# Kernel optimization log

Measured on AMD Instinct MI355X. Metric: run time of the kernel, lower is better.

The kernel has to match this reference:

```python
import jax, jax.numpy as jnp
import numpy as np

INPUT_SIZE = 1024
HEAD_SIZE = 64


def setup_inputs() -> dict:
    key = jax.random.key(0)
    kx, kk, kq, kv = jax.random.split(key, 4)
    B, T, C, H = 4, 4096, INPUT_SIZE, HEAD_SIZE
    x = jax.random.normal(kx, (B, T, C), dtype=jnp.float32)
    # nn.Linear(C, H, bias=False) weight is (H, C); we store transposed (C, H)
    # so that y = x @ W matches torch's x @ weight.T
    scale = 1.0 / np.sqrt(C)
    Wk = jax.random.uniform(kk, (C, H), dtype=jnp.float32, minval=-scale, maxval=scale)
    Wq = jax.random.uniform(kq, (C, H), dtype=jnp.float32, minval=-scale, maxval=scale)
    Wv = jax.random.uniform(kv, (C, H), dtype=jnp.float32, minval=-scale, maxval=scale)
    return {"x": x, "Wk": Wk, "Wq": Wq, "Wv": Wv}


def reference(x, Wk, Wq, Wv):
    B, T, C = x.shape
    k = x @ Wk  # (B, T, H)
    q = x @ Wq
    v = x @ Wv
    H = k.shape[-1]
    # scaled scores (B, T, T)
    wei = jnp.einsum('bth,bsh->bts', q, k) * (H ** -0.5)
    causal = jnp.tril(jnp.ones((T, T), dtype=bool))
    wei = jnp.where(causal, wei, -jnp.inf)
    wei = jax.nn.softmax(wei, axis=-1)
    out = jnp.einsum('bts,bsh->bth', wei, v)  # (B, T, H)
    return out
```

## Files before the change

kernel.cpp:

```cpp
#include <hip/hip_runtime.h>
#include <math.h>


#define BT   16384
#define TDIM 4096
#define CDIM 1024
#define HDIM 64
#define ACCW 68
#define NSLOT 288

typedef __attribute__((ext_vector_type(8))) short bf16x8;
typedef __attribute__((ext_vector_type(4))) float f32x4;
typedef __attribute__((ext_vector_type(8))) unsigned short us8;
typedef __attribute__((ext_vector_type(4))) unsigned short us4;

static __device__ __forceinline__ unsigned short f2bf(float f) {
    unsigned int u = __float_as_uint(f);
    u += 0x7fffu + ((u >> 16) & 1u);
    return (unsigned short)(u >> 16);
}

static __device__ __forceinline__ void pswap(unsigned &x, unsigned &y) {
    asm("v_permlane32_swap_b32 %0, %1" : "+v"(x), "+v"(y));
    asm("v_permlane16_swap_b32 %0, %1" : "+v"(x), "+v"(y));
}

__global__ __launch_bounds__(256) void wtrans(
    const float* __restrict__ Wk, const float* __restrict__ Wq,
    const float* __restrict__ Wv, unsigned short* __restrict__ wtg)
{
    int idx = blockIdx.x * 256 + threadIdx.x;
    int mat = idx >> 16;
    int rem = idx & 65535;
    int h = rem >> 10, c = rem & 1023;
    const float* W = (mat == 0) ? Wk : (mat == 1) ? Wq : Wv;
    wtg[idx] = f2bf(W[c * HDIM + h]);
}

__global__ __launch_bounds__(512) void qkv_proj(
    const float* __restrict__ x, const unsigned short* __restrict__ wtg,
    unsigned short* __restrict__ kg, unsigned short* __restrict__ qg,
    unsigned short* __restrict__ vtg)
{
    __shared__ __align__(16) unsigned short xs[2][32][72];
    __shared__ __align__(16) unsigned short wts[2][192][72];
    const int t = threadIdx.x;
    const int lane = t & 63, wv = t >> 6, quad = lane >> 4, l16 = lane & 15;
    const int mt = wv >> 2;
    const int nq = wv & 3;
    const int row0 = blockIdx.x * 32;

    const int xr = t >> 4, xc4 = (t & 15) * 4;
    const int wn = t >> 3, wc8 = (t & 7) * 8;

    f32x4 acc3[3];
    #pragma unroll
    for (int i = 0; i < 3; i++) acc3[i] = (f32x4){0.f, 0.f, 0.f, 0.f};

    const size_t xrow = (size_t)(row0 + xr) * CDIM + xc4;

    float4 xq[8];
    #pragma unroll
    for (int c = 0; c < 8; c++)
        xq[c] = *(const float4*)&x[xrow + c * 64];

    us8 w0 = *(const us8*)&wtg[(size_t)(wn +   0) * CDIM + wc8];
    us8 w1 = *(const us8*)&wtg[(size_t)(wn +  64) * CDIM + wc8];
    us8 w2 = *(const us8*)&wtg[(size_t)(wn + 128) * CDIM + wc8];

    {
        us4 pk = { f2bf(xq[0].x), f2bf(xq[0].y), f2bf(xq[0].z), f2bf(xq[0].w) };
        *(us4*)&xs[0][xr][xc4] = pk;
        *(us8*)&wts[0][wn +   0][wc8] = w0;
        *(us8*)&wts[0][wn +  64][wc8] = w1;
        *(us8*)&wts[0][wn + 128][wc8] = w2;
    }
    xq[0] = *(const float4*)&x[xrow + 8 * 64];
    w0 = *(const us8*)&wtg[(size_t)(wn +   0) * CDIM + 64 + wc8];
    w1 = *(const us8*)&wtg[(size_t)(wn +  64) * CDIM + 64 + wc8];
    w2 = *(const us8*)&wtg[(size_t)(wn + 128) * CDIM + 64 + wc8];
    __syncthreads();

    #pragma unroll
    for (int it = 0; it < 16; it++) {
        const int buf = it & 1;
        if (it + 1 < 16) {
            const int sl = (it + 1) & 7;
            us4 pk = { f2bf(xq[sl].x), f2bf(xq[sl].y),
                       f2bf(xq[sl].z), f2bf(xq[sl].w) };
            *(us4*)&xs[buf ^ 1][xr][xc4] = pk;
            *(us8*)&wts[buf ^ 1][wn +   0][wc8] = w0;
            *(us8*)&wts[buf ^ 1][wn +  64][wc8] = w1;
            *(us8*)&wts[buf ^ 1][wn + 128][wc8] = w2;
            if (it + 9 < 16)
                xq[sl] = *(const float4*)&x[xrow + (it + 9) * 64];
            if (it + 2 < 16) {
                int nc = (it + 2) * 64;
                w0 = *(const us8*)&wtg[(size_t)(wn +   0) * CDIM + nc + wc8];
                w1 = *(const us8*)&wtg[(size_t)(wn +  64) * CDIM + nc + wc8];
                w2 = *(const us8*)&wtg[(size_t)(wn + 128) * CDIM + nc + wc8];
            }
        }
        bf16x8 a0 = *(const bf16x8*)&xs[buf][mt * 16 + l16][quad * 8];
        bf16x8 a1 = *(const bf16x8*)&xs[buf][mt * 16 + l16][32 + quad * 8];
        #pragma unroll
        for (int j = 0; j < 3; j++) {
            int nt = nq * 3 + j;
            bf16x8 b0 = *(const bf16x8*)&wts[buf][nt * 16 + l16][quad * 8];
            bf16x8 b1 = *(const bf16x8*)&wts[buf][nt * 16 + l16][32 + quad * 8];
            acc3[j] = __builtin_amdgcn_mfma_f32_16x16x32_bf16(a0, b0, acc3[j], 0, 0, 0);
            acc3[j] = __builtin_amdgcn_mfma_f32_16x16x32_bf16(a1, b1, acc3[j], 0, 0, 0);
        }
        __syncthreads();
    }

    const int mrow = row0 + mt * 16 + quad * 4;
    #pragma unroll
    for (int j = 0; j < 3; j++) {
        int nt = nq * 3 + j;
        int mat = nt >> 2;
        int col = (nt & 3) * 16 + l16;
        if (mat == 2) {
            int bb = mrow >> 12, tr = mrow & 4095;
            us4 pv = { f2bf(acc3[j][0]), f2bf(acc3[j][1]),
                       f2bf(acc3[j][2]), f2bf(acc3[j][3]) };
            *(us4*)&vtg[((size_t)(bb * HDIM + col) << 12) + tr] = pv;
        } else {
            float s = (mat == 1) ? 0.125f : 1.0f;
            unsigned short* dst = (mat == 0) ? kg : qg;
            #pragma unroll
            for (int reg = 0; reg < 4; reg++)
                dst[(size_t)(mrow + reg) * HDIM + col] = f2bf(acc3[j][reg] * s);
        }
    }
}

__global__ __launch_bounds__(256) void attn(
    const unsigned short* __restrict__ qg, const unsigned short* __restrict__ kg,
    const unsigned short* __restrict__ vtg, float* __restrict__ slabs)
{
    __shared__ __align__(16) unsigned short Ks[2][64][72];
    __shared__ __align__(16) unsigned short Vt[2][64][72];

    const int t = threadIdx.x;
    const int lane = t & 63, wv = t >> 6, quad = lane >> 4, l16 = lane & 15;

    const int b = blockIdx.x / NSLOT;
    const int s = blockIdx.x - b * NSLOT;
    int a;
    if      (s < 8)   a = 0;
    else if (s < 24)  a = 1;
    else if (s < 48)  a = 2;
    else if (s < 80)  a = 3;
    else if (s < 120) a = 4;
    else if (s < 168) a = 5;
    else if (s < 224) a = 6;
    else              a = 7;
    const int u  = s - 4 * a * (a + 1);
    const int qt = a * 8 + u / (a + 1);
    const int c  = u % (a + 1);

    const size_t bbase = (size_t)b * TDIM;
    const int Q0 = qt * 64;
    const int kt0 = c * 8;
    const int kt1 = (kt0 + 7 < qt) ? kt0 + 7 : qt;

    const int qrow = Q0 + wv * 16 + l16;
    const bf16x8 qa0 = *(const bf16x8*)&qg[(bbase + qrow) * HDIM + quad * 8];
    const bf16x8 qa1 = *(const bf16x8*)&qg[(bbase + qrow) * HDIM + 32 + quad * 8];

    const short onev = (l16 == 0) ? (short)0x3F80 : (short)0;
    const bf16x8 ones = { onev, onev, onev, onev, onev, onev, onev, onev };

    f32x4 O[5];
    #pragma unroll
    for (int i = 0; i < 5; i++) O[i] = (f32x4){0.f, 0.f, 0.f, 0.f};

    const int fr = t >> 3, fc = (t & 7) * 8;

    us8 kr0 = *(const us8*)&kg[(bbase + kt0 * 64 + fr) * HDIM + fc];
    us8 kr1 = *(const us8*)&kg[(bbase + kt0 * 64 + fr + 32) * HDIM + fc];
    us8 vr0 = *(const us8*)&vtg[((size_t)(b * HDIM + fr) << 12) + kt0 * 64 + fc];
    us8 vr1 = *(const us8*)&vtg[((size_t)(b * HDIM + fr + 32) << 12) + kt0 * 64 + fc];
    *(us8*)&Ks[0][fr][fc] = kr0;
    *(us8*)&Ks[0][fr + 32][fc] = kr1;
    *(us8*)&Vt[0][fr][fc] = vr0;
    *(us8*)&Vt[0][fr + 32][fc] = vr1;
    if (kt0 < kt1) {
        int kn = kt0 + 1;
        kr0 = *(const us8*)&kg[(bbase + kn * 64 + fr) * HDIM + fc];
        kr1 = *(const us8*)&kg[(bbase + kn * 64 + fr + 32) * HDIM + fc];
        vr0 = *(const us8*)&vtg[((size_t)(b * HDIM + fr) << 12) + kn * 64 + fc];
        vr1 = *(const us8*)&vtg[((size_t)(b * HDIM + fr + 32) << 12) + kn * 64 + fc];
    }
    __syncthreads();

    const int qloc = wv * 16 + l16;
    int buf = 0;
    for (int kt = kt0; kt <= kt1; kt++) {
        __builtin_amdgcn_s_setprio(1);
        f32x4 sT[4];
        #pragma unroll
        for (int st = 0; st < 4; st++) {
            bf16x8 kb0 = *(const bf16x8*)&Ks[buf][st * 16 + l16][quad * 8];
            bf16x8 kb1 = *(const bf16x8*)&Ks[buf][st * 16 + l16][32 + quad * 8];
            f32x4 z = (f32x4){0.f, 0.f, 0.f, 0.f};
            z = __builtin_amdgcn_mfma_f32_16x16x32_bf16(kb0, qa0, z, 0, 0, 0);
            z = __builtin_amdgcn_mfma_f32_16x16x32_bf16(kb1, qa1, z, 0, 0, 0);
            sT[st] = z;
        }
        __builtin_amdgcn_s_setprio(0);

        if (kt < kt1) {
            *(us8*)&Ks[buf ^ 1][fr][fc] = kr0;
            *(us8*)&Ks[buf ^ 1][fr + 32][fc] = kr1;
            *(us8*)&Vt[buf ^ 1][fr][fc] = vr0;
            *(us8*)&Vt[buf ^ 1][fr + 32][fc] = vr1;
            if (kt + 1 < kt1) {
                int kn = kt + 2;
                kr0 = *(const us8*)&kg[(bbase + kn * 64 + fr) * HDIM + fc];
                kr1 = *(const us8*)&kg[(bbase + kn * 64 + fr + 32) * HDIM + fc];
                vr0 = *(const us8*)&vtg[((size_t)(b * HDIM + fr) << 12) + kn * 64 + fc];
                vr1 = *(const us8*)&vtg[((size_t)(b * HDIM + fr + 32) << 12) + kn * 64 + fc];
            }
        }

        float p[4][4];
        if (kt == qt) {
            #pragma unroll
            for (int st = 0; st < 4; st++)
                #pragma unroll
                for (int r = 0; r < 4; r++) {
                    int kkloc = st * 16 + quad * 4 + r;
                    p[st][r] = (kkloc > qloc) ? 0.f : __expf(sT[st][r]);
                }
        } else {
            #pragma unroll
            for (int st = 0; st < 4; st++)
                #pragma unroll
                for (int r = 0; r < 4; r++)
                    p[st][r] = __expf(sT[st][r]);
        }

        unsigned cpk[4][2];
        #pragma unroll
        for (int st = 0; st < 4; st++) {
            asm("v_cvt_pk_bf16_f32 %0, %1, %2"
                : "=v"(cpk[st][0]) : "v"(p[st][0]), "v"(p[st][1]));
            asm("v_cvt_pk_bf16_f32 %0, %1, %2"
                : "=v"(cpk[st][1]) : "v"(p[st][2]), "v"(p[st][3]));
        }
        union { unsigned u[4]; bf16x8 v; } pa0u, pa1u;
        {
            unsigned a0 = cpk[0][0], b0 = cpk[1][0]; pswap(a0, b0);
            unsigned a1 = cpk[0][1], b1 = cpk[1][1]; pswap(a1, b1);
            pa0u.u[0] = a0; pa0u.u[1] = a1; pa0u.u[2] = b0; pa0u.u[3] = b1;
            unsigned a2 = cpk[2][0], b2 = cpk[3][0]; pswap(a2, b2);
            unsigned a3 = cpk[2][1], b3 = cpk[3][1]; pswap(a3, b3);
            pa1u.u[0] = a2; pa1u.u[1] = a3; pa1u.u[2] = b2; pa1u.u[3] = b3;
        }
        const bf16x8 pa0 = pa0u.v, pa1 = pa1u.v;

        __builtin_amdgcn_s_setprio(1);
        #pragma unroll
        for (int nt = 0; nt < 4; nt++) {
            bf16x8 vb0 = *(const bf16x8*)&Vt[buf][nt * 16 + l16][quad * 8];
            bf16x8 vb1 = *(const bf16x8*)&Vt[buf][nt * 16 + l16][32 + quad * 8];
            O[nt] = __builtin_amdgcn_mfma_f32_16x16x32_bf16(pa0, vb0, O[nt], 0, 0, 0);
            O[nt] = __builtin_amdgcn_mfma_f32_16x16x32_bf16(pa1, vb1, O[nt], 0, 0, 0);
        }
        O[4] = __builtin_amdgcn_mfma_f32_16x16x32_bf16(pa0, ones, O[4], 0, 0, 0);
        O[4] = __builtin_amdgcn_mfma_f32_16x16x32_bf16(pa1, ones, O[4], 0, 0, 0);
        __builtin_amdgcn_s_setprio(0);

        __syncthreads();
        buf ^= 1;
    }

    float* slab = slabs + (size_t)(b * NSLOT + s) * 64 * ACCW;
    const int rl = wv * 16 + quad * 4;
    #pragma unroll
    for (int nt = 0; nt < 4; nt++)
        #pragma unroll
        for (int r = 0; r < 4; r++)
            slab[(size_t)(rl + r) * ACCW + nt * 16 + l16] = O[nt][r];
    if (l16 == 0) {
        #pragma unroll
        for (int r = 0; r < 4; r++)
            slab[(size_t)(rl + r) * ACCW + 64] = O[4][r];
    }
}

__global__ __launch_bounds__(256) void reduce_norm(
    const float* __restrict__ slabs, float* __restrict__ out)
{
    int idx = blockIdx.x * 256 + threadIdx.x;
    int row = idx >> 4, c4 = (idx & 15) * 4;
    int b = row >> 12, qt = (row >> 6) & 63, r64 = row & 63;
    int a = qt >> 3, nc = a + 1;
    int base = 4 * a * (a + 1) + (qt & 7) * nc;

    const float* sl = slabs + ((size_t)(b * NSLOT + base) * 64 + r64) * ACCW;
    float4 o = make_float4(0.f, 0.f, 0.f, 0.f);
    float l = 0.f;
    for (int i = 0; i < nc; i++) {
        float4 v = *(const float4*)&sl[c4];
        o.x += v.x; o.y += v.y; o.z += v.z; o.w += v.w;
        l += sl[64];
        sl += (size_t)64 * ACCW;
    }
    float inv = 1.f / l;
    *(float4*)&out[(size_t)row * HDIM + c4] =
        make_float4(o.x * inv, o.y * inv, o.z * inv, o.w * inv);
}

extern "C" void kernel_launch(void* const* d_in, const int* in_sizes, int n_in,
                              void* d_out, int out_size, void* d_ws, size_t ws_size,
                              hipStream_t stream) {
    const float* x  = (const float*)d_in[0];
    const float* Wk = (const float*)d_in[1];
    const float* Wq = (const float*)d_in[2];
    const float* Wv = (const float*)d_in[3];
    float* out = (float*)d_out;

    unsigned short* wtg = (unsigned short*)d_ws;
    unsigned short* kg  = wtg + 196608;
    unsigned short* qg  = kg + (size_t)BT * HDIM;
    unsigned short* vtg = qg + (size_t)BT * HDIM;
    float* slabs = (float*)(vtg + (size_t)4 * HDIM * TDIM);

    wtrans<<<768, 256, 0, stream>>>(Wk, Wq, Wv, wtg);
    qkv_proj<<<BT / 32, 512, 0, stream>>>(x, wtg, kg, qg, vtg);
    attn<<<4 * NSLOT, 256, 0, stream>>>(qg, kg, vtg, slabs);
    reduce_norm<<<BT * HDIM / (4 * 256), 256, 0, stream>>>(slabs, out);
}
```

Before: 141.7 us.

## Software-pipeline attention loop so QK^T of next tile overlaps softmax and PV

Restructures the key-tile loop into a prologue/steady-state/epilogue pipeline: the QK^T MFMAs for tile kt+1 are issued in the same block as the PV MFMAs for tile kt, and the exp/pack softmax step for the next tile runs after them. This is meant to let the exp and permlane VALU work interleave with matrix-core work instead of serialising per tile. It adds an extra barrier per iteration after the LDS stores and keeps more live registers (sT plus pa0/pa1), which could pressure occupancy.

Result: faster. 138.3 us, median of 2 (-2.3%).

```diff
diff --git a/kernel.cpp b/kernel.cpp
--- a/kernel.cpp
+++ b/kernel.cpp
@@ -23,6 +23,44 @@
 static __device__ __forceinline__ void pswap(unsigned &x, unsigned &y) {
     asm("v_permlane32_swap_b32 %0, %1" : "+v"(x), "+v"(y));
     asm("v_permlane16_swap_b32 %0, %1" : "+v"(x), "+v"(y));
+}
+
+static __device__ __forceinline__ void softmax_pack(
+    const f32x4 sT[4], bool diag, int qloc, int quad,
+    bf16x8 &pa0, bf16x8 &pa1)
+{
+    float p[4][4];
+    if (diag) {
+        #pragma unroll
+        for (int st = 0; st < 4; st++)
+            #pragma unroll
+            for (int r = 0; r < 4; r++) {
+                int kkloc = st * 16 + quad * 4 + r;
+                p[st][r] = (kkloc > qloc) ? 0.f : __expf(sT[st][r]);
+            }
+    } else {
+        #pragma unroll
+        for (int st = 0; st < 4; st++)
+            #pragma unroll
+            for (int r = 0; r < 4; r++)
+                p[st][r] = __expf(sT[st][r]);
+    }
+    unsigned cpk[4][2];
+    #pragma unroll
+    for (int st = 0; st < 4; st++) {
+        asm("v_cvt_pk_bf16_f32 %0, %1, %2"
+            : "=v"(cpk[st][0]) : "v"(p[st][0]), "v"(p[st][1]));
+        asm("v_cvt_pk_bf16_f32 %0, %1, %2"
+            : "=v"(cpk[st][1]) : "v"(p[st][2]), "v"(p[st][3]));
+    }
+    union { unsigned u[4]; bf16x8 v; } u0, u1;
+    unsigned a0 = cpk[0][0], b0 = cpk[1][0]; pswap(a0, b0);
+    unsigned a1 = cpk[0][1], b1 = cpk[1][1]; pswap(a1, b1);
+    u0.u[0] = a0; u0.u[1] = a1; u0.u[2] = b0; u0.u[3] = b1;
+    unsigned a2 = cpk[2][0], b2 = cpk[3][0]; pswap(a2, b2);
+    unsigned a3 = cpk[2][1], b3 = cpk[3][1]; pswap(a3, b3);
+    u1.u[0] = a2; u1.u[1] = a3; u1.u[2] = b2; u1.u[3] = b3;
+    pa0 = u0.v; pa1 = u1.v;
 }
 
 __global__ __launch_bounds__(256) void wtrans(
@@ -196,72 +234,48 @@
     __syncthreads();
 
     const int qloc = wv * 16 + l16;
-    int buf = 0;
-    for (int kt = kt0; kt <= kt1; kt++) {
-        __builtin_amdgcn_s_setprio(1);
+
+    bf16x8 pa0, pa1;
+    {
         f32x4 sT[4];
         #pragma unroll
         for (int st = 0; st < 4; st++) {
-            bf16x8 kb0 = *(const bf16x8*)&Ks[buf][st * 16 + l16][quad * 8];
-            bf16x8 kb1 = *(const bf16x8*)&Ks[buf][st * 16 + l16][32 + quad * 8];
+            bf16x8 kb0 = *(const bf16x8*)&Ks[0][st * 16 + l16][quad * 8];
+            bf16x8 kb1 = *(const bf16x8*)&Ks[0][st * 16 + l16][32 + quad * 8];
             f32x4 z = (f32x4){0.f, 0.f, 0.f, 0.f};
             z = __builtin_amdgcn_mfma_f32_16x16x32_bf16(kb0, qa0, z, 0, 0, 0);
             z = __builtin_amdgcn_mfma_f32_16x16x32_bf16(kb1, qa1, z, 0, 0, 0);
             sT[st] = z;
         }
-        __builtin_amdgcn_s_setprio(0);
-
-        if (kt < kt1) {
-            *(us8*)&Ks[buf ^ 1][fr][fc] = kr0;
-            *(us8*)&Ks[buf ^ 1][fr + 32][fc] = kr1;
-            *(us8*)&Vt[buf ^ 1][fr][fc] = vr0;
-            *(us8*)&Vt[buf ^ 1][fr + 32][fc] = vr1;
-            if (kt + 1 < kt1) {
-                int kn = kt + 2;
-                kr0 = *(const us8*)&kg[(bbase + kn * 64 + fr) * HDIM + fc];
-                kr1 = *(const us8*)&kg[(bbase + kn * 64 + fr + 32) * HDIM + fc];
-                vr0 = *(const us8*)&vtg[((size_t)(b * HDIM + fr) << 12) + kn * 64 + fc];
-                vr1 = *(const us8*)&vtg[((size_t)(b * HDIM + fr + 32) << 12) + kn * 64 + fc];
-            }
-        }
-
-        float p[4][4];
-        if (kt == qt) {
-            #pragma unroll
-            for (int st = 0; st < 4; st++)
-                #pragma unroll
-                for (int r = 0; r < 4; r++) {
-                    int kkloc = st * 16 + quad * 4 + r;
-                    p[st][r] = (kkloc > qloc) ? 0.f : __expf(sT[st][r]);
-                }
-        } else {
-            #pragma unroll
-            for (int st = 0; st < 4; st++)
-                #pragma unroll
-                for (int r = 0; r < 4; r++)
-                    p[st][r] = __expf(sT[st][r]);
-        }
-
-        unsigned cpk[4][2];
+        softmax_pack(sT, kt0 == qt, qloc, quad, pa0, pa1);
+    }
+
+    int buf = 0;
+    for (int kt = kt0; kt < kt1; ++kt) {
+        *(us8*)&Ks[buf ^ 1][fr][fc] = kr0;
+        *(us8*)&Ks[buf ^ 1][fr + 32][fc] = kr1;
+        *(us8*)&Vt[buf ^ 1][fr][fc] = vr0;
+        *(us8*)&Vt[buf ^ 1][fr + 32][fc] = vr1;
+        if (kt + 2 <= kt1) {
+            int kn = kt + 2;
+            kr0 = *(const us8*)&kg[(bbase + kn * 64 + fr) * HDIM + fc];
+            kr1 = *(const us8*)&kg[(bbase + kn * 64 + fr + 32) * HDIM + fc];
+            vr0 = *(const us8*)&vtg[((size_t)(b * HDIM + fr) << 12) + kn * 64 + fc];
+            vr1 = *(const us8*)&vtg[((size_t)(b * HDIM + fr + 32) << 12) + kn * 64 + fc];
+        }
+        __syncthreads();
+
+        __builtin_amdgcn_s_setprio(1);
+        f32x4 sT[4];
         #pragma unroll
         for (int st = 0; st < 4; st++) {
-            asm("v_cvt_pk_bf16_f32 %0, %1, %2"
-                : "=v"(cpk[st][0]) : "v"(p[st][0]), "v"(p[st][1]));
-            asm("v_cvt_pk_bf16_f32 %0, %1, %2"
-                : "=v"(cpk[st][1]) : "v"(p[st][2]), "v"(p[st][3]));
-        }
-        union { unsigned u[4]; bf16x8 v; } pa0u, pa1u;
-        {
-            unsigned a0 = cpk[0][0], b0 = cpk[1][0]; pswap(a0, b0);
-            unsigned a1 = cpk[0][1], b1 = cpk[1][1]; pswap(a1, b1);
-            pa0u.u[0] = a0; pa0u.u[1] = a1; pa0u.u[2] = b0; pa0u.u[3] = b1;
-            unsigned a2 = cpk[2][0], b2 = cpk[3][0]; pswap(a2, b2);
-            unsigned a3 = cpk[2][1], b3 = cpk[3][1]; pswap(a3, b3);
-            pa1u.u[0] = a2; pa1u.u[1] = a3; pa1u.u[2] = b2; pa1u.u[3] = b3;
-        }
-        const bf16x8 pa0 = pa0u.v, pa1 = pa1u.v;
-
-        __builtin_amdgcn_s_setprio(1);
+            bf16x8 kb0 = *(const bf16x8*)&Ks[buf ^ 1][st * 16 + l16][quad * 8];
+            bf16x8 kb1 = *(const bf16x8*)&Ks[buf ^ 1][st * 16 + l16][32 + quad * 8];
+            f32x4 z = (f32x4){0.f, 0.f, 0.f, 0.f};
+            z = __builtin_amdgcn_mfma_f32_16x16x32_bf16(kb0, qa0, z, 0, 0, 0);
+            z = __builtin_amdgcn_mfma_f32_16x16x32_bf16(kb1, qa1, z, 0, 0, 0);
+            sT[st] = z;
+        }
         #pragma unroll
         for (int nt = 0; nt < 4; nt++) {
             bf16x8 vb0 = *(const bf16x8*)&Vt[buf][nt * 16 + l16][quad * 8];
@@ -273,9 +287,21 @@
         O[4] = __builtin_amdgcn_mfma_f32_16x16x32_bf16(pa1, ones, O[4], 0, 0, 0);
         __builtin_amdgcn_s_setprio(0);
 
+        softmax_pack(sT, (kt + 1) == qt, qloc, quad, pa0, pa1);
+
         __syncthreads();
         buf ^= 1;
     }
+
+    #pragma unroll
+    for (int nt = 0; nt < 4; nt++) {
+        bf16x8 vb0 = *(const bf16x8*)&Vt[buf][nt * 16 + l16][quad * 8];
+        bf16x8 vb1 = *(const bf16x8*)&Vt[buf][nt * 16 + l16][32 + quad * 8];
+        O[nt] = __builtin_amdgcn_mfma_f32_16x16x32_bf16(pa0, vb0, O[nt], 0, 0, 0);
+        O[nt] = __builtin_amdgcn_mfma_f32_16x16x32_bf16(pa1, vb1, O[nt], 0, 0, 0);
+    }
+    O[4] = __builtin_amdgcn_mfma_f32_16x16x32_bf16(pa0, ones, O[4], 0, 0, 0);
+    O[4] = __builtin_amdgcn_mfma_f32_16x16x32_bf16(pa1, ones, O[4], 0, 0, 0);
 
     float* slab = slabs + (size_t)(b * NSLOT + s) * 64 * ACCW;
     const int rl = wv * 16 + quad * 4;
```
